# Performance work log

Hardware: AMD Instinct MI355X
Metric: run time of the kernel (lower is better)

Reference implementation:

```python
import jax, jax.numpy as jnp
import numpy as np
import math

B, S, D_MODEL, HEADS, GRID = 4, 2048, 512, 8, 8
HEAD_DIM = D_MODEL // HEADS
A_C, K_C, C_C = 0.9724108095811765, 0.9884401790754128, 0.999449553483052


def setup_inputs() -> dict:
    key = jax.random.key(0)
    ks = jax.random.split(key, 4)
    q = jax.random.normal(ks[0], (B, S, D_MODEL), jnp.float32)
    mask = jnp.tril(jnp.ones((S, S), dtype=bool))[None, None]  # causal (1,1,S,S)
    out_dim = 3 * D_MODEL
    grid_norm = jnp.arange(1, GRID + 1, dtype=jnp.float32)  # (grid,)
    # is_first=True init: normal(0,0.4)/output_dim/grid_norm_factor
    amplitudes = jax.random.normal(ks[1], (out_dim, D_MODEL, GRID), jnp.float32) * 0.4 / out_dim / grid_norm
    # norm_freq with is_first=True -> freq = arange(1..grid) / (grid+1)**0 = arange
    freq = jnp.arange(1, GRID + 1, dtype=jnp.float32)  # (grid,)
    grid_phase = jnp.arange(1, GRID + 1, dtype=jnp.float32) / (GRID + 1)
    input_phase = jnp.linspace(0.0, math.pi, D_MODEL, dtype=jnp.float32)[:, None]  # (in,1)
    phase0 = grid_phase[None, :] + input_phase  # (in, grid)
    ratio = 1.0
    for i in range(1, GRID):
        ratio *= A_C * i ** (-K_C) + C_C
    phase = phase0 * np.float32(ratio)
    kan_bias = jnp.ones((out_dim,), jnp.float32) / out_dim
    lim = math.sqrt(6.0 / (D_MODEL + D_MODEL))  # xavier_uniform
    out_w = jax.random.uniform(ks[2], (D_MODEL, D_MODEL), jnp.float32, -lim, lim)
    out_b = jnp.zeros((D_MODEL,), jnp.float32)
    return {"q": q, "mask": mask, "freq": freq, "phase": phase,
            "amplitudes": amplitudes, "kan_bias": kan_bias,
            "out_w": out_w, "out_b": out_b}


def sinekan(x2d, freq, phase, amp, bias):
    # y[n,j] = sum_{k,l} sin(x[n,k]*f[l] + p[k,l]) * amp[j,k,l] + bias[j]
    # expand sin(a+p) = sin(a)cos(p) + cos(a)sin(p); fold phase into weights
    ang = x2d[:, :, None] * freq  # (N, in, grid)
    w_sin = amp * jnp.cos(phase)  # (out, in, grid)
    w_cos = amp * jnp.sin(phase)
    y = (jnp.einsum('nkl,jkl->nj', jnp.sin(ang), w_sin)
         + jnp.einsum('nkl,jkl->nj', jnp.cos(ang), w_cos))
    return y + bias


def rotate_half(u):
    u1, u2 = jnp.split(u, 2, axis=-1)
    return jnp.concatenate([-u2, u1], axis=-1)


def apply_rope(x, pos_emb):
    cos, sin = jnp.split(pos_emb, 2, axis=-1)  # each (S, head_dim//2)
    x_even, x_odd = x[..., ::2], x[..., 1::2]
    x1 = x_even * cos + rotate_half(x_odd) * sin
    x2 = x_odd * cos + rotate_half(x_even) * sin
    return jnp.concatenate([x1, x2], axis=-1)


def rope_emb(seq_len, dim):
    half = dim // 2
    inv_freq = 1.0 / (10000.0 ** (jnp.arange(half, dtype=jnp.float32) / half))
    ang = jnp.arange(seq_len, dtype=jnp.float32)[:, None] * inv_freq  # (S, half)
    return jnp.concatenate([jnp.cos(ang), jnp.sin(ang)], axis=-1)  # (S, dim)


def reference(q, mask, freq, phase, amplitudes, kan_bias, out_w, out_b):
    b, s, _ = q.shape
    qkv = sinekan(q.reshape(-1, D_MODEL), freq, phase, amplitudes, kan_bias)
    qkv = qkv.reshape(b, s, HEADS, 3 * HEAD_DIM).transpose(0, 2, 1, 3)  # (b,h,s,3d)
    qs, ks, vs = jnp.split(qkv, 3, axis=-1)
    pe = rope_emb(s, HEAD_DIM)
    qs = apply_rope(qs, pe)
    ks = apply_rope(ks, pe)
    scores = jnp.einsum('bhqd,bhkd->bhqk', qs, ks) / math.sqrt(HEAD_DIM)
    scores = jnp.where(mask, scores.astype(jnp.float32), -1e9)
    attn = jax.nn.softmax(scores, axis=-1)
    ctx = jnp.einsum('bhqk,bhkd->bhqd', attn, vs)
    ctx = ctx.transpose(0, 2, 1, 3).reshape(b, s, D_MODEL)
    return ctx @ out_w.T + out_b
```

## Files before the change

### kernel.cpp

```cpp
#include <hip/hip_runtime.h>
#include <math.h>


typedef __attribute__((ext_vector_type(8))) short bf16x8;
typedef __attribute__((ext_vector_type(8))) unsigned short ushort8;
typedef __attribute__((ext_vector_type(4))) float f32x4;

#define DEV __device__ __forceinline__

DEV unsigned short f2bf(float f) {
  unsigned u = __builtin_bit_cast(unsigned, f);
  u += 0x7FFFu + ((u >> 16) & 1u);
  return (unsigned short)(u >> 16);
}
DEV float bf2f(unsigned short h) {
  unsigned u = ((unsigned)h) << 16;
  return __builtin_bit_cast(float, u);
}

#define GLDS16(gp, lp)                                                         \
  __builtin_amdgcn_global_load_lds(                                            \
      (const __attribute__((address_space(1))) void*)(gp),                     \
      (__attribute__((address_space(3))) void*)(lp), 16, 0, 0)

__global__ __launch_bounds__(256) void wprep(const float* __restrict__ amp,
                                             const float* __restrict__ phase,
                                             unsigned short* __restrict__ Wb) {
  int id = blockIdx.x * 256 + threadIdx.x;
  int j = id >> 9;
  int k = id & 511;
  const float* ap = amp + (size_t)id * 8;
  const float* ph = phase + k * 8;
  union { unsigned short u[16]; uint4 v[2]; } pk;
#pragma unroll
  for (int l = 0; l < 8; ++l) {
    float sp, cp;
    sincosf(ph[l], &sp, &cp);
    float a = ap[l];
    pk.u[l] = f2bf(a * cp);
    pk.u[8 + l] = f2bf(a * sp);
  }
  uint4* dst = (uint4*)(Wb + (size_t)j * 8192 + k * 16);
  dst[0] = pk.v[0];
  dst[1] = pk.v[1];
}

__global__ __launch_bounds__(256) void owprep(const float* __restrict__ w,
                                              unsigned short* __restrict__ o) {
  int id = blockIdx.x * 256 + threadIdx.x;
  o[id] = f2bf(w[id]);
}

__global__ __launch_bounds__(256) void fgen(const float* __restrict__ q,
                                            unsigned short* __restrict__ F) {
  int id = blockIdx.x * 256 + threadIdx.x;
  int row = id >> 9;
  int dim = id & 511;
  float x = q[(size_t)row * 512 + dim];
  float s1, c1;
  sincosf(x, &s1, &c1);
  union { unsigned short u[16]; uint4 v[2]; } fr;
  float s = s1, c = c1;
  fr.u[0] = f2bf(s);
  fr.u[8] = f2bf(c);
#pragma unroll
  for (int l = 1; l < 8; ++l) {
    float ns = s * c1 + c * s1;
    float nc = c * c1 - s * s1;
    s = ns; c = nc;
    fr.u[l] = f2bf(s);
    fr.u[8 + l] = f2bf(c);
  }
  uint4* dst = (uint4*)(F + (size_t)row * 8192 + dim * 16);
  dst[0] = fr.v[0];
  dst[1] = fr.v[1];
}

__global__ __launch_bounds__(512, 2) void kan_gemm8(
    const unsigned short* __restrict__ F, const unsigned short* __restrict__ Wb,
    const float* __restrict__ bias, unsigned short* __restrict__ qkv) {
  __shared__ __align__(16) char LDS[114688];

  const int tid = threadIdx.x, lane = tid & 63, wid = tid >> 6;
  const int wm = wid >> 2, wn = wid & 3;
  const int l15 = lane & 15, kg = lane >> 4;

  int bid = blockIdx.x;
  int xcd = bid & 7, u = bid >> 3;
  const int m0 = (xcd * 4 + (u & 3)) * 256;
  const int n0 = (u >> 2) * 192;

  const int growl = wid * 8 + (lane >> 3);
  const int cswz = ((lane & 7) ^ (lane >> 3)) << 4;

  f32x4 acc[2][4][3] = {};
  bf16x8 af0[4][2], af1[4][2], bf[3][2];

#define STAGE_A(T, C)                                                           \
  GLDS16((const char*)F + (size_t)(m0 + (C)*64 + growl) * 16384 +               \
             (size_t)(T) * 128 + cswz,                                          \
         LDS + (((T)&1) * 32768 + (C)*8192 + wid * 1024))

#define STAGE_B(T, C)                                                           \
  GLDS16((const char*)Wb + (size_t)(n0 + (C)*64 + growl) * 16384 +              \
             (size_t)(T) * 128 + cswz,                                          \
         LDS + (65536 + ((T)&1) * 24576 + (C)*8192 + wid * 1024))

#define DSREAD_A(DST, T, MQ)                                                    \
  do {                                                                          \
    _Pragma("unroll") for (int mi = 0; mi < 4; ++mi)                            \
        _Pragma("unroll") for (int kk = 0; kk < 2; ++kk) {                      \
      int _r = (MQ)*128 + wm * 64 + mi * 16 + l15;                              \
      DST[mi][kk] = *(const bf16x8*)(LDS + ((T)&1) * 32768 + _r * 128 +         \
                                     (((kk * 4 + kg) ^ (l15 & 7)) << 4));       \
    }                                                                           \
  } while (0)

#define DSREAD_B(T)                                                             \
  do {                                                                          \
    _Pragma("unroll") for (int ni = 0; ni < 3; ++ni)                            \
        _Pragma("unroll") for (int kk = 0; kk < 2; ++kk) {                      \
      int _r = wn * 48 + ni * 16 + l15;                                         \
      bf[ni][kk] = *(const bf16x8*)(LDS + 65536 + ((T)&1) * 24576 + _r * 128 +  \
                                    (((kk * 4 + kg) ^ (l15 & 7)) << 4));        \
    }                                                                           \
  } while (0)

#define MFMAS(AF, MQ, NI0, NI1)                                                 \
  do {                                                                          \
    __builtin_amdgcn_s_setprio(1);                                              \
    _Pragma("unroll") for (int mi = 0; mi < 4; ++mi)                            \
        _Pragma("unroll") for (int ni = (NI0); ni <= (NI1); ++ni)               \
            _Pragma("unroll") for (int kk = 0; kk < 2; ++kk)                    \
                acc[MQ][mi][ni] = __builtin_amdgcn_mfma_f32_16x16x32_bf16(      \
                    AF[mi][kk], bf[ni][kk], acc[MQ][mi][ni], 0, 0, 0);          \
    __builtin_amdgcn_s_setprio(0);                                              \
  } while (0)

#define BAR __builtin_amdgcn_s_barrier()
#define VMW(N) asm volatile("s_waitcnt vmcnt(" #N ")" ::: "memory")
#define LGW                                                                     \
  do {                                                                          \
    asm volatile("s_waitcnt lgkmcnt(0)" ::: "memory");                          \
    __builtin_amdgcn_sched_barrier(0);                                          \
  } while (0)

  STAGE_A(0, 0); STAGE_A(0, 1);
  STAGE_B(0, 0); STAGE_B(0, 1); STAGE_B(0, 2);
  STAGE_A(0, 2); STAGE_A(0, 3);

#pragma unroll 2
  for (int t = 0; t < 127; ++t) {
    VMW(2); BAR;
    DSREAD_A(af0, t, 0); DSREAD_B(t);
    STAGE_A(t + 1, 0); STAGE_A(t + 1, 1);
    LGW; MFMAS(af0, 0, 0, 1);
    BAR;
    DSREAD_A(af1, t, 1);
    STAGE_B(t + 1, 0); STAGE_B(t + 1, 1);
    MFMAS(af0, 0, 2, 2);
    VMW(4); BAR;
    STAGE_B(t + 1, 2); STAGE_A(t + 1, 2);
    MFMAS(af1, 1, 0, 1);
    BAR;
    STAGE_A(t + 1, 3);
    MFMAS(af1, 1, 2, 2);
  }
  {
    const int t = 127;
    VMW(2); BAR;
    DSREAD_A(af0, t, 0); DSREAD_B(t);
    LGW; MFMAS(af0, 0, 0, 1);
    BAR;
    DSREAD_A(af1, t, 1);
    MFMAS(af0, 0, 2, 2);
    VMW(0); BAR;
    MFMAS(af1, 1, 0, 1);
    BAR;
    MFMAS(af1, 1, 2, 2);
  }

#pragma unroll
  for (int mq = 0; mq < 2; ++mq)
#pragma unroll
    for (int mi = 0; mi < 4; ++mi)
#pragma unroll
      for (int ni = 0; ni < 3; ++ni) {
        int row = m0 + mq * 128 + wm * 64 + mi * 16 + kg * 4;
        int col = n0 + wn * 48 + ni * 16 + l15;
        float bv = bias[col];
        f32x4 a = acc[mq][mi][ni];
#pragma unroll
        for (int j = 0; j < 4; ++j)
          qkv[(size_t)(row + j) * 1536 + col] = f2bf(a[j] + bv);
      }
#undef STAGE_A
#undef STAGE_B
#undef DSREAD_A
#undef DSREAD_B
#undef MFMAS
#undef BAR
#undef VMW
#undef LGW
}

__global__ __launch_bounds__(256) void rope_prep(const unsigned short* __restrict__ qkv,
                                                 unsigned short* __restrict__ Qr,
                                                 unsigned short* __restrict__ Kr) {
  int id = blockIdx.x * 256 + threadIdx.x;
  int i = id & 31;
  int row = id >> 5;
  int s = row & 2047;
  int bh = row >> 11;
  int b = bh >> 3, h = bh & 7;

  const unsigned short* base = qkv + ((size_t)(b * 2048 + s)) * 1536 + h * 192;

  float inv = exp2f(-(float)i * (13.287712379549449f / 32.0f));
  float ang = (float)s * inv;
  float sn, cs;
  sincosf(ang, &sn, &cs);

  int pi = (i < 16) ? i + 16 : i - 16;
  float sign = (i < 16) ? -1.f : 1.f;
  size_t orow = (size_t)row * 64;

  {
    const unsigned short* xp = base;
    float xe = bf2f(xp[2 * i]), xo = bf2f(xp[2 * i + 1]);
    float po = bf2f(xp[2 * pi + 1]), pe = bf2f(xp[2 * pi]);
    Qr[orow + i] = f2bf(xe * cs + sign * po * sn);
    Qr[orow + 32 + i] = f2bf(xo * cs + sign * pe * sn);
  }
  {
    const unsigned short* xp = base + 64;
    float xe = bf2f(xp[2 * i]), xo = bf2f(xp[2 * i + 1]);
    float po = bf2f(xp[2 * pi + 1]), pe = bf2f(xp[2 * pi]);
    Kr[orow + i] = f2bf(xe * cs + sign * po * sn);
    Kr[orow + 32 + i] = f2bf(xo * cs + sign * pe * sn);
  }
}

__global__ __launch_bounds__(256) void attn(const unsigned short* __restrict__ Qr,
                                            const unsigned short* __restrict__ Kr,
                                            const unsigned short* __restrict__ qkv,
                                            unsigned short* __restrict__ ctx) {
  __shared__ __align__(16) char KB[8192];
  __shared__ __align__(16) char VT[8192];
  __shared__ __align__(16) char PL[9216];

  const int tid = threadIdx.x;
  const int lane = tid & 63;
  const int w = tid >> 6;
  const int qp = blockIdx.x;
  const int bh = blockIdx.y;
  const int b = bh >> 3, h = bh & 7;
  const int qwL = qp * 64 + w * 16;
  const int qwH = (31 - qp) * 64 + w * 16;
  const int l15 = lane & 15, kg = lane >> 4;

  const unsigned short* QpL = Qr + ((size_t)bh * 2048 + qwL + l15) * 64 + kg * 8;
  const unsigned short* QpH = Qr + ((size_t)bh * 2048 + qwH + l15) * 64 + kg * 8;
  bf16x8 qfL0 = *(const bf16x8*)QpL;
  bf16x8 qfL1 = *(const bf16x8*)(QpL + 32);
  bf16x8 qfH0 = *(const bf16x8*)QpH;
  bf16x8 qfH1 = *(const bf16x8*)(QpH + 32);

  f32x4 octxL[4] = {}, octxH[4] = {};
  float denL[4] = {0.f, 0.f, 0.f, 0.f}, denH[4] = {0.f, 0.f, 0.f, 0.f};
  char* Pw = PL + w * 2304;

  const int skp = tid >> 3;
  const int sds = tid & 7;
  const int vd = tid & 63;
  const int vkq = tid >> 6;

#define QKPV(QF0, QF1, OCTX, DEN, QW)                                          \
  do {                                                                         \
    f32x4 zero = {0.f, 0.f, 0.f, 0.f};                                         \
    _Pragma("unroll") for (int f = 0; f < 4; ++f) {                            \
      int kp = f * 16 + l15;                                                   \
      int swk = (kp & 7) << 4;                                                 \
      bf16x8 kf0 = *(const bf16x8*)(KB + ((kp * 128 + kg * 16) ^ swk));        \
      bf16x8 kf1 = *(const bf16x8*)(KB + ((kp * 128 + 64 + kg * 16) ^ swk));   \
      f32x4 sA =                                                               \
          __builtin_amdgcn_mfma_f32_16x16x32_bf16(QF0, kf0, zero, 0, 0, 0);    \
      sA = __builtin_amdgcn_mfma_f32_16x16x32_bf16(QF1, kf1, sA, 0, 0, 0);     \
      int kgl = kt * 64 + kp;                                                  \
      _Pragma("unroll") for (int j = 0; j < 4; ++j) {                          \
        int qrow = (QW) + kg * 4 + j;                                          \
        float pp = (kgl <= qrow) ? __expf(sA[j] * 0.125f) : 0.f;               \
        DEN[j] += pp;                                                          \
        int prow = kg * 4 + j;                                                 \
        *(unsigned short*)(Pw + prow * 144 + kp * 2) = f2bf(pp);               \
      }                                                                        \
    }                                                                          \
    bf16x8 pf0 = *(const bf16x8*)(Pw + l15 * 144 + kg * 16);                   \
    bf16x8 pf1 = *(const bf16x8*)(Pw + l15 * 144 + 64 + kg * 16);              \
    _Pragma("unroll") for (int nd = 0; nd < 4; ++nd) {                         \
      int d = nd * 16 + l15;                                                   \
      int swv = (d & 7) << 4;                                                  \
      bf16x8 vf0 = *(const bf16x8*)(VT + (d * 128 + ((kg * 16) ^ swv)));       \
      bf16x8 vf1 = *(const bf16x8*)(VT + (d * 128 + ((64 + kg * 16) ^ swv)));  \
      OCTX[nd] =                                                               \
          __builtin_amdgcn_mfma_f32_16x16x32_bf16(pf0, vf0, OCTX[nd], 0, 0, 0);\
      OCTX[nd] =                                                               \
          __builtin_amdgcn_mfma_f32_16x16x32_bf16(pf1, vf1, OCTX[nd], 0, 0, 0);\
    }                                                                          \
  } while (0)

  const int nktH = 32 - qp;
  const int nktL = qp + 1;
  for (int kt = 0; kt < nktH; ++kt) {
#pragma unroll
    for (int r = 0; r < 2; ++r) {
      int krow = r * 32 + skp;
      ushort8 kv = *(const ushort8*)(Kr + ((size_t)bh * 2048 + kt * 64 + krow) * 64 +
                                     sds * 8);
      *(ushort8*)(KB + ((krow * 128 + sds * 16) ^ ((krow & 7) << 4))) = kv;
      const unsigned short* vcol =
          qkv + ((size_t)(b * 2048 + kt * 64 + r * 32 + vkq * 8)) * 1536 +
          h * 192 + 128 + vd;
      ushort8 vv;
#pragma unroll
      for (int jj = 0; jj < 8; ++jj) vv[jj] = vcol[jj * 1536];
      int slot = r * 4 + vkq;
      *(ushort8*)(VT + (vd * 128 + ((slot * 16) ^ ((vd & 7) << 4)))) = vv;
    }
    __syncthreads();

    QKPV(qfH0, qfH1, octxH, denH, qwH);
    if (kt < nktL) QKPV(qfL0, qfL1, octxL, denL, qwL);
    __syncthreads();
  }
#undef QKPV

#pragma unroll
  for (int j = 0; j < 4; ++j) {
    float dH = denH[j], dL = denL[j];
    dH += __shfl_xor(dH, 1); dL += __shfl_xor(dL, 1);
    dH += __shfl_xor(dH, 2); dL += __shfl_xor(dL, 2);
    dH += __shfl_xor(dH, 4); dL += __shfl_xor(dL, 4);
    dH += __shfl_xor(dH, 8); dL += __shfl_xor(dL, 8);
    denH[j] = dH; denL[j] = dL;
  }
#pragma unroll
  for (int nd = 0; nd < 4; ++nd)
#pragma unroll
    for (int j = 0; j < 4; ++j) {
      int col = h * 64 + nd * 16 + l15;
      int qrowH = qwH + kg * 4 + j;
      int qrowL = qwL + kg * 4 + j;
      ctx[((size_t)b * 2048 + qrowH) * 512 + col] = f2bf(octxH[nd][j] / denH[j]);
      ctx[((size_t)b * 2048 + qrowL) * 512 + col] = f2bf(octxL[nd][j] / denL[j]);
    }
}

__global__ __launch_bounds__(256) void out_gemm(const unsigned short* __restrict__ A,
                                                const unsigned short* __restrict__ Bw,
                                                const float* __restrict__ outb,
                                                float* __restrict__ out) {
  __shared__ __align__(16) unsigned short Al[128 * 32];
  __shared__ __align__(16) unsigned short Bl[128 * 32];
  const int tid = threadIdx.x, lane = tid & 63, w = tid >> 6;
  const int wm = w >> 1, wn = w & 1;
  const int m0 = blockIdx.x * 128, n0 = blockIdx.y * 128;
  const int l15 = lane & 15, kg = lane >> 4;

  f32x4 acc[4][4] = {};

  const unsigned short* ga = A + (size_t)(m0 + (tid >> 2)) * 512 + (tid & 3) * 8;
  const unsigned short* gb = Bw + (size_t)(n0 + (tid >> 2)) * 512 + (tid & 3) * 8;

  for (int t = 0; t < 16; ++t) {
    GLDS16(ga + t * 32, &Al[w * 512]);
    GLDS16(ga + t * 32 + 64 * 512, &Al[2048 + w * 512]);
    GLDS16(gb + t * 32, &Bl[w * 512]);
    GLDS16(gb + t * 32 + 64 * 512, &Bl[2048 + w * 512]);
    __syncthreads();

    bf16x8 af[4], bfr[4];
#pragma unroll
    for (int m = 0; m < 4; ++m)
      af[m] = *(const bf16x8*)&Al[(wm * 64 + m * 16 + l15) * 32 + kg * 8];
#pragma unroll
    for (int n = 0; n < 4; ++n)
      bfr[n] = *(const bf16x8*)&Bl[(wn * 64 + n * 16 + l15) * 32 + kg * 8];
#pragma unroll
    for (int m = 0; m < 4; ++m)
#pragma unroll
      for (int n = 0; n < 4; ++n)
        acc[m][n] =
            __builtin_amdgcn_mfma_f32_16x16x32_bf16(af[m], bfr[n], acc[m][n], 0, 0, 0);

    __syncthreads();
  }

  const int rb = m0 + wm * 64 + kg * 4;
  const int cb = n0 + wn * 64 + l15;
#pragma unroll
  for (int n = 0; n < 4; ++n) {
    int cc = cb + n * 16;
    float bv = outb[cc];
#pragma unroll
    for (int m = 0; m < 4; ++m)
#pragma unroll
      for (int j = 0; j < 4; ++j)
        out[(size_t)(rb + m * 16 + j) * 512 + cc] = acc[m][n][j] + bv;
  }
}

extern "C" void kernel_launch(void* const* d_in, const int* in_sizes, int n_in,
                              void* d_out, int out_size, void* d_ws, size_t ws_size,
                              hipStream_t stream) {
  const float* q = (const float*)d_in[0];
  const float* phase = (const float*)d_in[3];
  const float* amp = (const float*)d_in[4];
  const float* kbias = (const float*)d_in[5];
  const float* out_w = (const float*)d_in[6];
  const float* out_b = (const float*)d_in[7];
  float* out = (float*)d_out;

  char* p = (char*)d_ws;
  unsigned short* Wb = (unsigned short*)(p);
  unsigned short* qkv = (unsigned short*)(p + 25165824);
  unsigned short* Qr = (unsigned short*)(p + 50331648);
  unsigned short* Kr = (unsigned short*)(p + 58720256);
  unsigned short* ctx = (unsigned short*)(p + 67108864);
  unsigned short* Wob = (unsigned short*)(p + 75497472);
  unsigned short* F = (unsigned short*)(p + 76021760);

  owprep<<<1024, 256, 0, stream>>>(out_w, Wob);
  wprep<<<3072, 256, 0, stream>>>(amp, phase, Wb);
  fgen<<<16384, 256, 0, stream>>>(q, F);
  kan_gemm8<<<256, 512, 0, stream>>>(F, Wb, kbias, qkv);
  rope_prep<<<8192, 256, 0, stream>>>(qkv, Qr, Kr);
  attn<<<dim3(16, 32), 256, 0, stream>>>(Qr, Kr, qkv, ctx);
  out_gemm<<<dim3(64, 4), 256, 0, stream>>>(ctx, Wob, out_b, out);
}
```

Before: 289.2 us.

## Fuse sine/cosine feature generation into KAN GEMM A-operand staging

Removes the separate fgen kernel and its 128MB-per-pass bf16 feature matrix F. Each block of the KAN GEMM now computes sin/cos harmonics from q directly into swizzled LDS for the A tile, interleaved with the MFMA stages. This avoids writing and re-reading the large feature buffer from HBM. In exchange it adds sincos and transcendental work inside the GEMM loop, repeated across the 8 column blocks per row tile, and tightens waits to vmcnt(0)/lgkmcnt(0) each iteration.

```diff
diff --git a/kernel.cpp b/kernel.cpp
--- a/kernel.cpp
+++ b/kernel.cpp
@@ -51,33 +51,8 @@
   o[id] = f2bf(w[id]);
 }
 
-__global__ __launch_bounds__(256) void fgen(const float* __restrict__ q,
-                                            unsigned short* __restrict__ F) {
-  int id = blockIdx.x * 256 + threadIdx.x;
-  int row = id >> 9;
-  int dim = id & 511;
-  float x = q[(size_t)row * 512 + dim];
-  float s1, c1;
-  sincosf(x, &s1, &c1);
-  union { unsigned short u[16]; uint4 v[2]; } fr;
-  float s = s1, c = c1;
-  fr.u[0] = f2bf(s);
-  fr.u[8] = f2bf(c);
-#pragma unroll
-  for (int l = 1; l < 8; ++l) {
-    float ns = s * c1 + c * s1;
-    float nc = c * c1 - s * s1;
-    s = ns; c = nc;
-    fr.u[l] = f2bf(s);
-    fr.u[8 + l] = f2bf(c);
-  }
-  uint4* dst = (uint4*)(F + (size_t)row * 8192 + dim * 16);
-  dst[0] = fr.v[0];
-  dst[1] = fr.v[1];
-}
-
 __global__ __launch_bounds__(512, 2) void kan_gemm8(
-    const unsigned short* __restrict__ F, const unsigned short* __restrict__ Wb,
+    const float* __restrict__ q, const unsigned short* __restrict__ Wb,
     const float* __restrict__ bias, unsigned short* __restrict__ qkv) {
   __shared__ __align__(16) char LDS[114688];
 
@@ -93,18 +68,38 @@
   const int growl = wid * 8 + (lane >> 3);
   const int cswz = ((lane & 7) ^ (lane >> 3)) << 4;
 
+  const int fr_ = tid >> 1;
+  const int fd_ = (tid & 1) * 2;
+  const float* qrow = q + (size_t)(m0 + fr_) * 512;
+
   f32x4 acc[2][4][3] = {};
   bf16x8 af0[4][2], af1[4][2], bf[3][2];
-
-#define STAGE_A(T, C)                                                           \
-  GLDS16((const char*)F + (size_t)(m0 + (C)*64 + growl) * 16384 +               \
-             (size_t)(T) * 128 + cswz,                                          \
-         LDS + (((T)&1) * 32768 + (C)*8192 + wid * 1024))
 
 #define STAGE_B(T, C)                                                           \
   GLDS16((const char*)Wb + (size_t)(n0 + (C)*64 + growl) * 16384 +              \
              (size_t)(T) * 128 + cswz,                                          \
          LDS + (65536 + ((T)&1) * 24576 + (C)*8192 + wid * 1024))
+
+#define FEAT(T, S, X)                                                           \
+  do {                                                                          \
+    float s1_, c1_;                                                             \
+    sincosf((X), &s1_, &c1_);                                                   \
+    union { unsigned short u[16]; uint4 v[2]; } fr2;                            \
+    float s_ = s1_, c_ = c1_;                                                   \
+    fr2.u[0] = f2bf(s_);                                                        \
+    fr2.u[8] = f2bf(c_);                                                        \
+    _Pragma("unroll") for (int l = 1; l < 8; ++l) {                             \
+      float ns_ = s_ * c1_ + c_ * s1_;                                          \
+      float nc_ = c_ * c1_ - s_ * s1_;                                          \
+      s_ = ns_; c_ = nc_;                                                       \
+      fr2.u[l] = f2bf(s_);                                                      \
+      fr2.u[8 + l] = f2bf(c_);                                                  \
+    }                                                                           \
+    int dl_ = fd_ + (S);                                                        \
+    char* dst_ = LDS + (((T)&1) * 32768) + fr_ * 128;                           \
+    *(uint4*)(dst_ + (((2 * dl_) ^ (fr_ & 7)) << 4)) = fr2.v[0];                \
+    *(uint4*)(dst_ + (((2 * dl_ + 1) ^ (fr_ & 7)) << 4)) = fr2.v[1];            \
+  } while (0)
 
 #define DSREAD_A(DST, T, MQ)                                                    \
   do {                                                                          \
@@ -139,42 +134,47 @@
 
 #define BAR __builtin_amdgcn_s_barrier()
 #define VMW(N) asm volatile("s_waitcnt vmcnt(" #N ")" ::: "memory")
+#define LGK0 asm volatile("s_waitcnt lgkmcnt(0)" ::: "memory")
 #define LGW                                                                     \
   do {                                                                          \
-    asm volatile("s_waitcnt lgkmcnt(0)" ::: "memory");                          \
+    LGK0;                                                                       \
     __builtin_amdgcn_sched_barrier(0);                                          \
   } while (0)
 
-  STAGE_A(0, 0); STAGE_A(0, 1);
+  {
+    float2 xq0 = *(const float2*)(qrow + fd_);
+    FEAT(0, 0, xq0.x);
+    FEAT(0, 1, xq0.y);
+  }
   STAGE_B(0, 0); STAGE_B(0, 1); STAGE_B(0, 2);
-  STAGE_A(0, 2); STAGE_A(0, 3);
-
+
+  float2 xq;
 #pragma unroll 2
   for (int t = 0; t < 127; ++t) {
-    VMW(2); BAR;
+    VMW(0); LGK0; BAR;
     DSREAD_A(af0, t, 0); DSREAD_B(t);
-    STAGE_A(t + 1, 0); STAGE_A(t + 1, 1);
+    xq = *(const float2*)(qrow + 4 * (t + 1) + fd_);
+    STAGE_B(t + 1, 0); STAGE_B(t + 1, 1); STAGE_B(t + 1, 2);
     LGW; MFMAS(af0, 0, 0, 1);
     BAR;
     DSREAD_A(af1, t, 1);
-    STAGE_B(t + 1, 0); STAGE_B(t + 1, 1);
+    FEAT(t + 1, 0, xq.x);
     MFMAS(af0, 0, 2, 2);
-    VMW(4); BAR;
-    STAGE_B(t + 1, 2); STAGE_A(t + 1, 2);
+    BAR;
+    FEAT(t + 1, 1, xq.y);
     MFMAS(af1, 1, 0, 1);
     BAR;
-    STAGE_A(t + 1, 3);
     MFMAS(af1, 1, 2, 2);
   }
   {
     const int t = 127;
-    VMW(2); BAR;
+    VMW(0); LGK0; BAR;
     DSREAD_A(af0, t, 0); DSREAD_B(t);
     LGW; MFMAS(af0, 0, 0, 1);
     BAR;
     DSREAD_A(af1, t, 1);
     MFMAS(af0, 0, 2, 2);
-    VMW(0); BAR;
+    BAR;
     MFMAS(af1, 1, 0, 1);
     BAR;
     MFMAS(af1, 1, 2, 2);
@@ -194,13 +194,14 @@
         for (int j = 0; j < 4; ++j)
           qkv[(size_t)(row + j) * 1536 + col] = f2bf(a[j] + bv);
       }
-#undef STAGE_A
 #undef STAGE_B
+#undef FEAT
 #undef DSREAD_A
 #undef DSREAD_B
 #undef MFMAS
 #undef BAR
 #undef VMW
+#undef LGK0
 #undef LGW
 }
 
@@ -428,12 +429,10 @@
   unsigned short* Kr = (unsigned short*)(p + 58720256);
   unsigned short* ctx = (unsigned short*)(p + 67108864);
   unsigned short* Wob = (unsigned short*)(p + 75497472);
-  unsigned short* F = (unsigned short*)(p + 76021760);
 
   owprep<<<1024, 256, 0, stream>>>(out_w, Wob);
   wprep<<<3072, 256, 0, stream>>>(amp, phase, Wb);
-  fgen<<<16384, 256, 0, stream>>>(q, F);
-  kan_gemm8<<<256, 512, 0, stream>>>(F, Wb, kbias, qkv);
+  kan_gemm8<<<256, 512, 0, stream>>>(q, Wb, kbias, qkv);
   rope_prep<<<8192, 256, 0, stream>>>(qkv, Qr, Kr);
   attn<<<dim3(16, 32), 256, 0, stream>>>(Qr, Kr, qkv, ctx);
   out_gemm<<<dim3(64, 4), 256, 0, stream>>>(ctx, Wob, out_b, out);
```

Result: slower. 359.1 us (+24.2%).
